# Performance work log

Measured on AMD Instinct MI355X. Metric: run time of the kernel, lower is better.

Reference implementation:

```python
import jax, jax.numpy as jnp
import numpy as np
import math

N_VERT = 35709
N_FACE = 70789
BATCH = 32


def _normalize(x, axis=-1, eps=1e-12):
    n = jnp.linalg.norm(x, axis=axis, keepdims=True)
    return x / jnp.maximum(n, eps)


def setup_inputs() -> dict:
    key = jax.random.key(0)
    ks = jax.random.split(key, 9)
    coeff = jax.random.normal(ks[0], (BATCH, 277), jnp.float32)
    idBase = jax.random.normal(ks[1], (3 * N_VERT, 80), jnp.float32)
    exBase = jax.random.normal(ks[2], (3 * N_VERT, 64), jnp.float32)
    texBase = jax.random.normal(ks[3], (3 * N_VERT, 100), jnp.float32)
    meanshape = jax.random.normal(ks[4], (3 * N_VERT,), jnp.float32)
    meantex = jax.random.normal(ks[5], (3 * N_VERT,), jnp.float32)
    face_buf = jax.random.randint(ks[6], (N_FACE, 3), 0, N_VERT, jnp.int32)
    # point_buf may index the appended zero-normal row at position N_FACE (padding)
    point_buf = jax.random.randint(ks[7], (N_VERT, 8), 0, N_FACE + 1, jnp.int32)
    keypoints = jax.random.randint(ks[8], (68,), 0, N_VERT, jnp.int32)
    return dict(coeff=coeff, idBase=idBase, exBase=exBase, texBase=texBase,
                meanshape=meanshape, meantex=meantex, face_buf=face_buf,
                point_buf=point_buf, keypoints=keypoints)


def reference(coeff, idBase, exBase, texBase, meanshape, meantex,
              face_buf, point_buf, keypoints):
    B = coeff.shape[0]
    # ---- Split_coeff (canonical 80/64/100/3/27/3 layout) ----
    id_c = coeff[:, :80]
    ex_c = coeff[:, 80:144]
    tex_c = coeff[:, 144:244]
    angles = coeff[:, 244:247]
    gamma = coeff[:, 247:274]
    trans = coeff[:, 274:277]
    cam_scale = jnp.ones((B, 1), coeff.dtype)
    f_scale = jnp.ones((B, 1), coeff.dtype)

    # ---- Shape formation ----
    fs = (jnp.einsum('ij,aj->ai', idBase, id_c)
          + jnp.einsum('ij,aj->ai', exBase, ex_c)
          + meanshape[None, :])
    fs = fs.reshape(B, -1, 3)  # [B, N, 3]
    fs = fs - jnp.mean(meanshape.reshape(-1, 3), axis=0)[None, None, :]

    # ---- Texture formation ----
    tex = (jnp.einsum('ij,aj->ai', texBase, tex_c) + meantex[None, :]).reshape(B, -1, 3)

    # ---- Rotation matrix (Rz @ Ry @ Rx, then transpose) ----
    cx, sx = jnp.cos(angles[:, 0]), jnp.sin(angles[:, 0])
    cy, sy = jnp.cos(angles[:, 1]), jnp.sin(angles[:, 1])
    cz, sz = jnp.cos(angles[:, 2]), jnp.sin(angles[:, 2])
    o, z = jnp.ones_like(cx), jnp.zeros_like(cx)
    Rx = jnp.stack([o, z, z, z, cx, -sx, z, sx, cx], -1).reshape(B, 3, 3)
    Ry = jnp.stack([cy, z, sy, z, o, z, -sy, z, cy], -1).reshape(B, 3, 3)
    Rz = jnp.stack([cz, -sz, z, sz, cz, z, z, z, o], -1).reshape(B, 3, 3)
    rot = jnp.swapaxes(jnp.matmul(jnp.matmul(Rz, Ry), Rx), 1, 2)  # [B,3,3]

    # ---- Compute_norm: gather face verts, cross, aggregate to vertices ----
    v1 = fs[:, face_buf[:, 0], :]  # [B, F, 3]
    v2 = fs[:, face_buf[:, 1], :]
    v3 = fs[:, face_buf[:, 2], :]
    face_norm = _normalize(jnp.cross(v1 - v2, v2 - v3), axis=2)  # [B, F, 3]
    face_norm = jnp.concatenate(
        [face_norm, jnp.zeros((B, 1, 3), face_norm.dtype)], axis=1)  # pad row
    v_norm = _normalize(jnp.sum(face_norm[:, point_buf, :], axis=2), axis=2)  # [B,N,3]

    norm_r = jnp.matmul(v_norm, rot)

    # ---- Rigid transform + landmarks ----
    fst = jnp.matmul(fs, rot) + trans[:, None, :]
    lm = fst[:, keypoints, :]  # [B, 68, 3]

    # ---- Projection block (applied to landmarks) ----
    focal = 1015.0 * f_scale  # [B,1]
    camera_pos = jnp.array([0.0, 0.0, 10.0], coeff.dtype) * cam_scale[:, :, None]  # [B,1,3]
    reverse_z = jnp.diag(jnp.array([1.0, 1.0, -1.0], coeff.dtype))
    z1 = jnp.zeros((B, 1), coeff.dtype)
    z2 = jnp.zeros((B, 2), coeff.dtype)
    o1 = jnp.ones((B, 1), coeff.dtype)
    p_matrix = jnp.concatenate(
        [focal, z1, 112.0 * o1, z1, focal, 112.0 * o1, z2, o1], axis=1).reshape(B, 3, 3)
    lm_cam = jnp.matmul(lm, reverse_z[None]) + camera_pos
    aug = jnp.matmul(lm_cam, jnp.swapaxes(p_matrix, 1, 2))
    landmark_p = aug[..., :2] / aug[..., 2:3]

    # ---- SH illumination ----
    init_lit = jnp.array([0.8, 0, 0, 0, 0, 0, 0, 0, 0], coeff.dtype)
    g = gamma.reshape(B, 3, 9) + init_lit[None, None, :]
    pi = math.pi
    a0, a1, a2 = pi, 2 * pi / math.sqrt(3.0), 2 * pi / math.sqrt(8.0)
    c0 = 1.0 / math.sqrt(4 * pi)
    c1 = math.sqrt(3.0) / math.sqrt(4 * pi)
    c2 = 3 * math.sqrt(5.0) / math.sqrt(12 * pi)
    nx, ny, nz = norm_r[..., 0], norm_r[..., 1], norm_r[..., 2]
    Y = jnp.stack([
        a0 * c0 * jnp.ones_like(nx),
        -a1 * c1 * ny,
        a1 * c1 * nz,
        -a1 * c1 * nx,
        a2 * c2 * nx * ny,
        -a2 * c2 * ny * nz,
        a2 * c2 * 0.5 / math.sqrt(3.0) * (3 * nz * nz - 1),
        -a2 * c2 * nx * nz,
        a2 * c2 * 0.5 * (nx * nx - ny * ny),
    ], axis=-1)  # [B, N, 9]
    lighting = jnp.einsum('bnk,bck->bnc', Y, g)  # [B, N, 3]
    face_color = tex * lighting

    return face_color, landmark_p, fst
```

## Files before the change

### kernel.cpp

```cpp
#include <hip/hip_runtime.h>

#define N_VERT 35709
#define N_FACE 70789
#define NB 32
#define M3 (3*N_VERT)

#define WS_FS4X  ((size_t)0)
#define WS_FN4X  (WS_FS4X + (size_t)N_VERT*128)
#define WS_CPAD  (WS_FN4X + (size_t)(N_FACE+1)*128)
#define WS_ROT   (WS_CPAD + (size_t)NB*256)
#define WS_TRE   (WS_ROT + (size_t)NB*9)
#define WS_G     (WS_TRE + (size_t)NB*3)
#define WS_MEAN  (WS_G + (size_t)NB*27)

#define FC_OFF   ((size_t)0)
#define LM_OFF   ((size_t)NB*M3)
#define FST_OFF  (LM_OFF + (size_t)NB*68*2)

#define A0C0 0.88622692545275801f
#define A1C1 1.77245385090551603f
#define A2C2 2.42703239430f
#define Y6C  0.70062393935f
#define Y8C  1.21351619715f

__global__ void __launch_bounds__(256) face3d_stageA1(
    const float* __restrict__ ms, float* __restrict__ ws) {
  float s0=0.f, s1=0.f, s2=0.f;
  for (int v = blockIdx.x*256 + threadIdx.x; v < N_VERT; v += gridDim.x*256) {
    s0 += ms[3*v+0]; s1 += ms[3*v+1]; s2 += ms[3*v+2];
  }
  #pragma unroll
  for (int off = 32; off > 0; off >>= 1) {
    s0 += __shfl_down(s0, off);
    s1 += __shfl_down(s1, off);
    s2 += __shfl_down(s2, off);
  }
  if ((threadIdx.x & 63) == 0) {
    atomicAdd(&ws[WS_MEAN+0], s0);
    atomicAdd(&ws[WS_MEAN+1], s1);
    atomicAdd(&ws[WS_MEAN+2], s2);
  }
}

__global__ void __launch_bounds__(256) face3d_stageA2(
    const float* __restrict__ coeff, float* __restrict__ ws) {
  int t = threadIdx.x;
  float m0 = ws[WS_MEAN+0]*(1.0f/N_VERT);
  float m1 = ws[WS_MEAN+1]*(1.0f/N_VERT);
  float m2 = ws[WS_MEAN+2]*(1.0f/N_VERT);
  float4* cp4 = (float4*)(ws + WS_CPAD);
  for (int idx = t; idx < 64*32; idx += 256) {
    int s4 = idx >> 5, b = idx & 31;
    int k = 4*s4;
    float4 v;
    v.x = (k < 244) ? coeff[b*277 + k + 0] : 0.f;
    v.y = (k < 244) ? coeff[b*277 + k + 1] : 0.f;
    v.z = (k < 244) ? coeff[b*277 + k + 2] : 0.f;
    v.w = (k < 244) ? coeff[b*277 + k + 3] : 0.f;
    cp4[idx] = v;
  }
  for (int idx = t; idx < NB*27; idx += 256) {
    int b = idx / 27, k = idx - b*27;
    ws[WS_G + idx] = coeff[b*277 + 247 + k] + (((k % 9) == 0) ? 0.8f : 0.0f);
  }
  if (t < NB) {
    int b = t;
    float ax = coeff[b*277+244], ay = coeff[b*277+245], az = coeff[b*277+246];
    float cx=cosf(ax), sx=sinf(ax);
    float cy=cosf(ay), sy=sinf(ay);
    float cz=cosf(az), sz=sinf(az);
    float T00=cz*cy, T01=-sz, T02=cz*sy;
    float T10=sz*cy, T11=cz,  T12=sz*sy;
    float T20=-sy,   T21=0.f, T22=cy;
    float R[3][3];
    R[0][0]=T00; R[0][1]=T01*cx+T02*sx; R[0][2]=-T01*sx+T02*cx;
    R[1][0]=T10; R[1][1]=T11*cx+T12*sx; R[1][2]=-T11*sx+T12*cx;
    R[2][0]=T20; R[2][1]=T21*cx+T22*sx; R[2][2]=-T21*sx+T22*cx;
    float rot[3][3];
    #pragma unroll
    for (int c=0;c<3;c++)
      #pragma unroll
      for (int j=0;j<3;j++)
        rot[c][j] = R[j][c];
    #pragma unroll
    for (int c=0;c<3;c++)
      #pragma unroll
      for (int j=0;j<3;j++)
        ws[WS_ROT + b*9 + c*3 + j] = rot[c][j];
    #pragma unroll
    for (int j=0;j<3;j++)
      ws[WS_TRE + b*3 + j] = coeff[b*277+274+j]
        - (m0*rot[0][j] + m1*rot[1][j] + m2*rot[2][j]);
  }
}


template<int NK4, int SOFF>
__device__ __forceinline__ void gemm2(const float4* __restrict__ A0,
                                      const float4* __restrict__ A1,
                                      const float4* __restrict__ Wl,
                                      float acc[2][NB]) {
  float4 c0 = A0[0], c1 = A1[0];
  #pragma unroll 1
  for (int s = 0; s < NK4; ++s) {
    float4 a0 = c0, a1 = c1;
    if (s + 1 < NK4) { c0 = A0[s+1]; c1 = A1[s+1]; }
    const float4* __restrict__ Ws = Wl + (size_t)(SOFF + s)*32;
    #pragma unroll
    for (int b = 0; b < NB; ++b) {
      float4 w = Ws[b];
      acc[0][b] = fmaf(a0.w, w.w, fmaf(a0.z, w.z, fmaf(a0.y, w.y, fmaf(a0.x, w.x, acc[0][b]))));
      acc[1][b] = fmaf(a1.w, w.w, fmaf(a1.z, w.z, fmaf(a1.y, w.y, fmaf(a1.x, w.x, acc[1][b]))));
    }
  }
}

__global__ void __launch_bounds__(128) face3d_stageB(
    const float* __restrict__ idB, const float* __restrict__ exB,
    const float* __restrict__ texB, const float* __restrict__ meanshape,
    const float* __restrict__ meantex, const float* __restrict__ cpadT,
    float* __restrict__ fs4x, float* __restrict__ texOut) {
  __shared__ float4 Wl[36*32];
  int t = threadIdx.x;
  int bid = blockIdx.x;
  int isTex = bid & 1;
  int r0 = (bid >> 1) * 256;

  const float4* __restrict__ cp4 = (const float4*)cpadT;
  if (!isTex) {
    #pragma unroll
    for (int i = 0; i < 9; ++i) Wl[t + 128*i] = cp4[t + 128*i];
  } else {
    for (int i = t; i < 25*32; i += 128) Wl[i] = cp4[36*32 + i];
  }
  __syncthreads();

  int ra = r0 + t;
  int rb = r0 + t + 128;
  int rac = (ra < M3) ? ra : (M3-1);
  int rbc = (rb < M3) ? rb : (M3-1);

  float acc[2][NB];
  #pragma unroll
  for (int j = 0; j < 2; ++j)
    #pragma unroll
    for (int b = 0; b < NB; ++b) acc[j][b] = 0.f;

  if (!isTex) {
    gemm2<20, 0 >((const float4*)idB + (size_t)rac*20,
                  (const float4*)idB + (size_t)rbc*20, Wl, acc);
    gemm2<16, 20>((const float4*)exB + (size_t)rac*16,
                  (const float4*)exB + (size_t)rbc*16, Wl, acc);
    #pragma unroll
    for (int j = 0; j < 2; ++j) {
      int r = (j == 0) ? ra : rb;
      if (r < M3) {
        float msv = meanshape[r];
        int v = r/3, c = r - 3*v;
        float* dst = fs4x + (size_t)v*128 + c;
        #pragma unroll
        for (int b = 0; b < NB; ++b) dst[b*4] = acc[j][b] + msv;
      }
    }
  } else {
    gemm2<25, 0 >((const float4*)texB + (size_t)rac*25,
                  (const float4*)texB + (size_t)rbc*25, Wl, acc);
    #pragma unroll
    for (int j = 0; j < 2; ++j) {
      int r = (j == 0) ? ra : rb;
      if (r < M3) {
        float mtv = meantex[r];
        #pragma unroll
        for (int b = 0; b < NB; ++b) texOut[(size_t)b*M3 + r] = acc[j][b] + mtv;
      }
    }
  }
}

__global__ void __launch_bounds__(256) face3d_stageC(
    const int* __restrict__ face_buf, const float* __restrict__ fs4x,
    float* __restrict__ fn4x) {
  int t = threadIdx.x;
  int b = t & 31, fi = t >> 5;
  int f = blockIdx.x*8 + fi;
  if (f > N_FACE) return;
  float4* o = (float4*)(fn4x + ((size_t)f*32 + b)*4);
  if (f == N_FACE) { *o = make_float4(0.f,0.f,0.f,0.f); return; }
  int i0 = face_buf[f*3+0];
  int i1 = face_buf[f*3+1];
  int i2 = face_buf[f*3+2];
  float4 p1 = *(const float4*)(fs4x + ((size_t)i0*32 + b)*4);
  float4 p2 = *(const float4*)(fs4x + ((size_t)i1*32 + b)*4);
  float4 p3 = *(const float4*)(fs4x + ((size_t)i2*32 + b)*4);
  float e1x = p1.x-p2.x, e1y = p1.y-p2.y, e1z = p1.z-p2.z;
  float e2x = p2.x-p3.x, e2y = p2.y-p3.y, e2z = p2.z-p3.z;
  float nx = e1y*e2z - e1z*e2y;
  float ny = e1z*e2x - e1x*e2z;
  float nz = e1x*e2y - e1y*e2x;
  float inv = 1.0f / fmaxf(sqrtf(nx*nx + ny*ny + nz*nz), 1e-12f);
  *o = make_float4(nx*inv, ny*inv, nz*inv, 0.f);
}

__global__ void __launch_bounds__(256) face3d_stageD(
    const int* __restrict__ point_buf, const int* __restrict__ keypoints,
    const float* __restrict__ fs4x, const float* __restrict__ fn4x,
    const float* __restrict__ rotAll, const float* __restrict__ treAll,
    const float* __restrict__ gAll, float* __restrict__ out) {
  const int mainBlocks = (N_VERT + 7)/8;
  int bid = blockIdx.x;
  int t = threadIdx.x;
  if (bid < mainBlocks) {
    __shared__ float rotL[NB*9];
    __shared__ float treL[NB*3];
    __shared__ float gL[NB*27];
    __shared__ float fstL[NB*33];
    __shared__ float LL[NB*33];
    if (t < NB*9)  rotL[t] = rotAll[t];
    if (t < NB*3)  treL[t] = treAll[t];
    for (int i = t; i < NB*27; i += 256) gL[i] = gAll[i];
    __syncthreads();
    int b = t & 31, vi = t >> 5;
    int v0 = bid*8;
    int v = v0 + vi;
    if (v < N_VERT) {
      const int4 pb0 = *(const int4*)(point_buf + (size_t)v*8);
      const int4 pb1 = *(const int4*)(point_buf + (size_t)v*8 + 4);
      float4 g0 = *(const float4*)(fn4x + ((size_t)pb0.x*32 + b)*4);
      float4 g1 = *(const float4*)(fn4x + ((size_t)pb0.y*32 + b)*4);
      float4 g2 = *(const float4*)(fn4x + ((size_t)pb0.z*32 + b)*4);
      float4 g3 = *(const float4*)(fn4x + ((size_t)pb0.w*32 + b)*4);
      float4 g4 = *(const float4*)(fn4x + ((size_t)pb1.x*32 + b)*4);
      float4 g5 = *(const float4*)(fn4x + ((size_t)pb1.y*32 + b)*4);
      float4 g6 = *(const float4*)(fn4x + ((size_t)pb1.z*32 + b)*4);
      float4 g7 = *(const float4*)(fn4x + ((size_t)pb1.w*32 + b)*4);
      float sx = ((g0.x+g1.x)+(g2.x+g3.x)) + ((g4.x+g5.x)+(g6.x+g7.x));
      float sy = ((g0.y+g1.y)+(g2.y+g3.y)) + ((g4.y+g5.y)+(g6.y+g7.y));
      float sz = ((g0.z+g1.z)+(g2.z+g3.z)) + ((g4.z+g5.z)+(g6.z+g7.z));
      float inv = 1.0f / fmaxf(sqrtf(sx*sx + sy*sy + sz*sz), 1e-12f);
      float n0 = sx*inv, n1 = sy*inv, n2 = sz*inv;
      const float* rot = rotL + b*9;
      float r00=rot[0], r01=rot[1], r02=rot[2];
      float r10=rot[3], r11=rot[4], r12=rot[5];
      float r20=rot[6], r21=rot[7], r22=rot[8];
      float nx = n0*r00 + n1*r10 + n2*r20;
      float ny = n0*r01 + n1*r11 + n2*r21;
      float nz = n0*r02 + n1*r12 + n2*r22;
      float Y1 = -A1C1*ny;
      float Y2 =  A1C1*nz;
      float Y3 = -A1C1*nx;
      float Y4 =  A2C2*nx*ny;
      float Y5 = -A2C2*ny*nz;
      float Y6 =  Y6C*(3.f*nz*nz - 1.f);
      float Y7 = -A2C2*nx*nz;
      float Y8 =  Y8C*(nx*nx - ny*ny);
      const float* g = gL + b*27;
      #pragma unroll
      for (int c = 0; c < 3; ++c) {
        const float* gc = g + c*9;
        float Lc = A0C0*gc[0] + Y1*gc[1] + Y2*gc[2] + Y3*gc[3] + Y4*gc[4]
                 + Y5*gc[5] + Y6*gc[6] + Y7*gc[7] + Y8*gc[8];
        LL[b*33 + vi*4 + c] = Lc;
      }
      float4 fsv = *(const float4*)(fs4x + ((size_t)v*32 + b)*4);
      const float* tre = treL + b*3;
      fstL[b*33 + vi*4 + 0] = fsv.x*r00 + fsv.y*r10 + fsv.z*r20 + tre[0];
      fstL[b*33 + vi*4 + 1] = fsv.x*r01 + fsv.y*r11 + fsv.z*r21 + tre[1];
      fstL[b*33 + vi*4 + 2] = fsv.x*r02 + fsv.y*r12 + fsv.z*r22 + tre[2];
    }
    __syncthreads();
    int b2 = t >> 3, w = t & 7;
    if (v0 + w < N_VERT) {
      size_t obase = (size_t)b2*M3 + (size_t)(v0 + w)*3;
      float f0 = fstL[b2*33 + w*4 + 0];
      float f1 = fstL[b2*33 + w*4 + 1];
      float f2 = fstL[b2*33 + w*4 + 2];
      out[FST_OFF + obase + 0] = f0;
      out[FST_OFF + obase + 1] = f1;
      out[FST_OFF + obase + 2] = f2;
      float l0 = LL[b2*33 + w*4 + 0];
      float l1 = LL[b2*33 + w*4 + 1];
      float l2 = LL[b2*33 + w*4 + 2];
      float t0 = out[FC_OFF + obase + 0];
      float t1 = out[FC_OFF + obase + 1];
      float t2 = out[FC_OFF + obase + 2];
      out[FC_OFF + obase + 0] = t0*l0;
      out[FC_OFF + obase + 1] = t1*l1;
      out[FC_OFF + obase + 2] = t2*l2;
    }
  } else {
    int idx = (bid - mainBlocks)*256 + t;
    if (idx >= NB*68) return;
    int b = idx & 31, j = idx >> 5;
    int kp = keypoints[j];
    const float* rot = rotAll + b*9;
    const float* tre = treAll + b*3;
    float4 fsv = *(const float4*)(fs4x + ((size_t)kp*32 + b)*4);
    float o0 = fsv.x*rot[0] + fsv.y*rot[3] + fsv.z*rot[6] + tre[0];
    float o1 = fsv.x*rot[1] + fsv.y*rot[4] + fsv.z*rot[7] + tre[1];
    float o2 = fsv.x*rot[2] + fsv.y*rot[5] + fsv.z*rot[8] + tre[2];
    float zc = 10.0f - o2;
    float axv = 1015.0f*o0 + 112.0f*zc;
    float ayv = 1015.0f*o1 + 112.0f*zc;
    out[LM_OFF + (size_t)b*136 + (size_t)j*2 + 0] = axv/zc;
    out[LM_OFF + (size_t)b*136 + (size_t)j*2 + 1] = ayv/zc;
  }
}

extern "C" void kernel_launch(void* const* d_in, const int* in_sizes, int n_in,
                              void* d_out, int out_size, void* d_ws, size_t ws_size,
                              hipStream_t stream) {
  const float* coeff     = (const float*)d_in[0];
  const float* idB       = (const float*)d_in[1];
  const float* exB       = (const float*)d_in[2];
  const float* texB      = (const float*)d_in[3];
  const float* meanshape = (const float*)d_in[4];
  const float* meantex   = (const float*)d_in[5];
  const int*   face_buf  = (const int*)d_in[6];
  const int*   point_buf = (const int*)d_in[7];
  const int*   keypoints = (const int*)d_in[8];
  float* out = (float*)d_out;
  float* ws  = (float*)d_ws;

  hipMemsetAsync((char*)d_ws + WS_MEAN*sizeof(float), 0, 3*sizeof(float), stream);

  hipLaunchKernelGGL(face3d_stageA1, dim3(56), dim3(256), 0, stream, meanshape, ws);
  hipLaunchKernelGGL(face3d_stageA2, dim3(1), dim3(256), 0, stream, coeff, ws);

  int gridB = 2 * ((M3 + 255)/256);
  hipLaunchKernelGGL(face3d_stageB, dim3(gridB), dim3(128), 0, stream,
                     idB, exB, texB, meanshape, meantex,
                     ws + WS_CPAD, ws + WS_FS4X, out + FC_OFF);

  int gridC = (N_FACE + 1 + 7)/8;
  hipLaunchKernelGGL(face3d_stageC, dim3(gridC), dim3(256), 0, stream,
                     face_buf, ws + WS_FS4X, ws + WS_FN4X);

  int mainBlocks = (N_VERT + 7)/8;
  int lmBlocks   = (NB*68 + 255)/256;
  hipLaunchKernelGGL(face3d_stageD, dim3(mainBlocks + lmBlocks), dim3(256), 0, stream,
                     point_buf, keypoints, ws + WS_FS4X, ws + WS_FN4X,
                     ws + WS_ROT, ws + WS_TRE, ws + WS_G, out);
}
```

Baseline: 278.2 us.

## Fuse face-normal computation into per-vertex normal kernel, drop stage C

Removes the separate face-normal kernel and its intermediate buffer. Each vertex thread now recomputes the normals of its 8 adjacent faces directly from the face indices and vertex positions. This saves one launch plus the write and re-read of a (N_FACE+1)x32 float4 buffer. In exchange it triples the random gathers per adjacent face (3 vertex float4 loads instead of 1 normal load) and repeats the cross-product work about 8x/2 times, since each face is shared by roughly 3.4 vertices.

```diff
diff --git a/kernel.cpp b/kernel.cpp
--- a/kernel.cpp
+++ b/kernel.cpp
@@ -177,33 +177,10 @@
   }
 }
 
-__global__ void __launch_bounds__(256) face3d_stageC(
-    const int* __restrict__ face_buf, const float* __restrict__ fs4x,
-    float* __restrict__ fn4x) {
-  int t = threadIdx.x;
-  int b = t & 31, fi = t >> 5;
-  int f = blockIdx.x*8 + fi;
-  if (f > N_FACE) return;
-  float4* o = (float4*)(fn4x + ((size_t)f*32 + b)*4);
-  if (f == N_FACE) { *o = make_float4(0.f,0.f,0.f,0.f); return; }
-  int i0 = face_buf[f*3+0];
-  int i1 = face_buf[f*3+1];
-  int i2 = face_buf[f*3+2];
-  float4 p1 = *(const float4*)(fs4x + ((size_t)i0*32 + b)*4);
-  float4 p2 = *(const float4*)(fs4x + ((size_t)i1*32 + b)*4);
-  float4 p3 = *(const float4*)(fs4x + ((size_t)i2*32 + b)*4);
-  float e1x = p1.x-p2.x, e1y = p1.y-p2.y, e1z = p1.z-p2.z;
-  float e2x = p2.x-p3.x, e2y = p2.y-p3.y, e2z = p2.z-p3.z;
-  float nx = e1y*e2z - e1z*e2y;
-  float ny = e1z*e2x - e1x*e2z;
-  float nz = e1x*e2y - e1y*e2x;
-  float inv = 1.0f / fmaxf(sqrtf(nx*nx + ny*ny + nz*nz), 1e-12f);
-  *o = make_float4(nx*inv, ny*inv, nz*inv, 0.f);
-}
-
 __global__ void __launch_bounds__(256) face3d_stageD(
-    const int* __restrict__ point_buf, const int* __restrict__ keypoints,
-    const float* __restrict__ fs4x, const float* __restrict__ fn4x,
+    const int* __restrict__ face_buf, const int* __restrict__ point_buf,
+    const int* __restrict__ keypoints,
+    const float* __restrict__ fs4x,
     const float* __restrict__ rotAll, const float* __restrict__ treAll,
     const float* __restrict__ gAll, float* __restrict__ out) {
   const int mainBlocks = (N_VERT + 7)/8;
@@ -225,17 +202,31 @@
     if (v < N_VERT) {
       const int4 pb0 = *(const int4*)(point_buf + (size_t)v*8);
       const int4 pb1 = *(const int4*)(point_buf + (size_t)v*8 + 4);
-      float4 g0 = *(const float4*)(fn4x + ((size_t)pb0.x*32 + b)*4);
-      float4 g1 = *(const float4*)(fn4x + ((size_t)pb0.y*32 + b)*4);
-      float4 g2 = *(const float4*)(fn4x + ((size_t)pb0.z*32 + b)*4);
-      float4 g3 = *(const float4*)(fn4x + ((size_t)pb0.w*32 + b)*4);
-      float4 g4 = *(const float4*)(fn4x + ((size_t)pb1.x*32 + b)*4);
-      float4 g5 = *(const float4*)(fn4x + ((size_t)pb1.y*32 + b)*4);
-      float4 g6 = *(const float4*)(fn4x + ((size_t)pb1.z*32 + b)*4);
-      float4 g7 = *(const float4*)(fn4x + ((size_t)pb1.w*32 + b)*4);
-      float sx = ((g0.x+g1.x)+(g2.x+g3.x)) + ((g4.x+g5.x)+(g6.x+g7.x));
-      float sy = ((g0.y+g1.y)+(g2.y+g3.y)) + ((g4.y+g5.y)+(g6.y+g7.y));
-      float sz = ((g0.z+g1.z)+(g2.z+g3.z)) + ((g4.z+g5.z)+(g6.z+g7.z));
+      int fk[8] = {pb0.x, pb0.y, pb0.z, pb0.w, pb1.x, pb1.y, pb1.z, pb1.w};
+      float nxk[8], nyk[8], nzk[8];
+      #pragma unroll
+      for (int k = 0; k < 8; ++k) {
+        int f = fk[k];
+        float rx = 0.f, ry = 0.f, rz = 0.f;
+        if (f != N_FACE) {
+          const int* fb = face_buf + (size_t)f*3;
+          int i0 = fb[0], i1 = fb[1], i2 = fb[2];
+          float4 p1 = *(const float4*)(fs4x + ((size_t)i0*32 + b)*4);
+          float4 p2 = *(const float4*)(fs4x + ((size_t)i1*32 + b)*4);
+          float4 p3 = *(const float4*)(fs4x + ((size_t)i2*32 + b)*4);
+          float e1x = p1.x-p2.x, e1y = p1.y-p2.y, e1z = p1.z-p2.z;
+          float e2x = p2.x-p3.x, e2y = p2.y-p3.y, e2z = p2.z-p3.z;
+          float cxv = e1y*e2z - e1z*e2y;
+          float cyv = e1z*e2x - e1x*e2z;
+          float czv = e1x*e2y - e1y*e2x;
+          float inv = 1.0f / fmaxf(sqrtf(cxv*cxv + cyv*cyv + czv*czv), 1e-12f);
+          rx = cxv*inv; ry = cyv*inv; rz = czv*inv;
+        }
+        nxk[k] = rx; nyk[k] = ry; nzk[k] = rz;
+      }
+      float sx = ((nxk[0]+nxk[1])+(nxk[2]+nxk[3])) + ((nxk[4]+nxk[5])+(nxk[6]+nxk[7]));
+      float sy = ((nyk[0]+nyk[1])+(nyk[2]+nyk[3])) + ((nyk[4]+nyk[5])+(nyk[6]+nyk[7]));
+      float sz = ((nzk[0]+nzk[1])+(nzk[2]+nzk[3])) + ((nzk[4]+nzk[5])+(nzk[6]+nzk[7]));
       float inv = 1.0f / fmaxf(sqrtf(sx*sx + sy*sy + sz*sz), 1e-12f);
       float n0 = sx*inv, n1 = sy*inv, n2 = sz*inv;
       const float* rot = rotL + b*9;
@@ -331,13 +322,9 @@
                      idB, exB, texB, meanshape, meantex,
                      ws + WS_CPAD, ws + WS_FS4X, out + FC_OFF);
 
-  int gridC = (N_FACE + 1 + 7)/8;
-  hipLaunchKernelGGL(face3d_stageC, dim3(gridC), dim3(256), 0, stream,
-                     face_buf, ws + WS_FS4X, ws + WS_FN4X);
-
   int mainBlocks = (N_VERT + 7)/8;
   int lmBlocks   = (NB*68 + 255)/256;
   hipLaunchKernelGGL(face3d_stageD, dim3(mainBlocks + lmBlocks), dim3(256), 0, stream,
-                     point_buf, keypoints, ws + WS_FS4X, ws + WS_FN4X,
+                     face_buf, point_buf, keypoints, ws + WS_FS4X,
                      ws + WS_ROT, ws + WS_TRE, ws + WS_G, out);
 }
```

New measurement: 289.7 us. 4.1% more time.

## Fuse texture GEMM into vertex stage and drop tex round-trip through output

Applied to the files above, without the earlier changes.

Removes the texture half of the basis GEMM kernel and instead computes each vertex's three texture rows inside the per-vertex lighting kernel, using tex coefficients staged in shared memory. This avoids writing the full batched texture to the output buffer and reading it back to multiply by lighting. In exchange the per-vertex kernel gains a 100-term dot product per thread and extra shared memory, which may reduce occupancy and GEMM efficiency.

```diff
diff --git a/kernel.cpp b/kernel.cpp
--- a/kernel.cpp
+++ b/kernel.cpp
@@ -117,22 +117,15 @@
 
 __global__ void __launch_bounds__(128) face3d_stageB(
     const float* __restrict__ idB, const float* __restrict__ exB,
-    const float* __restrict__ texB, const float* __restrict__ meanshape,
-    const float* __restrict__ meantex, const float* __restrict__ cpadT,
-    float* __restrict__ fs4x, float* __restrict__ texOut) {
+    const float* __restrict__ meanshape, const float* __restrict__ cpadT,
+    float* __restrict__ fs4x) {
   __shared__ float4 Wl[36*32];
   int t = threadIdx.x;
-  int bid = blockIdx.x;
-  int isTex = bid & 1;
-  int r0 = (bid >> 1) * 256;
+  int r0 = blockIdx.x * 256;
 
   const float4* __restrict__ cp4 = (const float4*)cpadT;
-  if (!isTex) {
-    #pragma unroll
-    for (int i = 0; i < 9; ++i) Wl[t + 128*i] = cp4[t + 128*i];
-  } else {
-    for (int i = t; i < 25*32; i += 128) Wl[i] = cp4[36*32 + i];
-  }
+  #pragma unroll
+  for (int i = 0; i < 9; ++i) Wl[t + 128*i] = cp4[t + 128*i];
   __syncthreads();
 
   int ra = r0 + t;
@@ -146,33 +139,19 @@
     #pragma unroll
     for (int b = 0; b < NB; ++b) acc[j][b] = 0.f;
 
-  if (!isTex) {
-    gemm2<20, 0 >((const float4*)idB + (size_t)rac*20,
-                  (const float4*)idB + (size_t)rbc*20, Wl, acc);
-    gemm2<16, 20>((const float4*)exB + (size_t)rac*16,
-                  (const float4*)exB + (size_t)rbc*16, Wl, acc);
-    #pragma unroll
-    for (int j = 0; j < 2; ++j) {
-      int r = (j == 0) ? ra : rb;
-      if (r < M3) {
-        float msv = meanshape[r];
-        int v = r/3, c = r - 3*v;
-        float* dst = fs4x + (size_t)v*128 + c;
-        #pragma unroll
-        for (int b = 0; b < NB; ++b) dst[b*4] = acc[j][b] + msv;
-      }
-    }
-  } else {
-    gemm2<25, 0 >((const float4*)texB + (size_t)rac*25,
-                  (const float4*)texB + (size_t)rbc*25, Wl, acc);
-    #pragma unroll
-    for (int j = 0; j < 2; ++j) {
-      int r = (j == 0) ? ra : rb;
-      if (r < M3) {
-        float mtv = meantex[r];
-        #pragma unroll
-        for (int b = 0; b < NB; ++b) texOut[(size_t)b*M3 + r] = acc[j][b] + mtv;
-      }
+  gemm2<20, 0 >((const float4*)idB + (size_t)rac*20,
+                (const float4*)idB + (size_t)rbc*20, Wl, acc);
+  gemm2<16, 20>((const float4*)exB + (size_t)rac*16,
+                (const float4*)exB + (size_t)rbc*16, Wl, acc);
+  #pragma unroll
+  for (int j = 0; j < 2; ++j) {
+    int r = (j == 0) ? ra : rb;
+    if (r < M3) {
+      float msv = meanshape[r];
+      int v = r/3, c = r - 3*v;
+      float* dst = fs4x + (size_t)v*128 + c;
+      #pragma unroll
+      for (int b = 0; b < NB; ++b) dst[b*4] = acc[j][b] + msv;
     }
   }
 }
@@ -204,6 +183,8 @@
 __global__ void __launch_bounds__(256) face3d_stageD(
     const int* __restrict__ point_buf, const int* __restrict__ keypoints,
     const float* __restrict__ fs4x, const float* __restrict__ fn4x,
+    const float* __restrict__ texB, const float* __restrict__ meantex,
+    const float* __restrict__ cpadT,
     const float* __restrict__ rotAll, const float* __restrict__ treAll,
     const float* __restrict__ gAll, float* __restrict__ out) {
   const int mainBlocks = (N_VERT + 7)/8;
@@ -215,9 +196,15 @@
     __shared__ float gL[NB*27];
     __shared__ float fstL[NB*33];
     __shared__ float LL[NB*33];
+    __shared__ float texL[NB*33];
+    __shared__ float4 Wt[25*32];
     if (t < NB*9)  rotL[t] = rotAll[t];
     if (t < NB*3)  treL[t] = treAll[t];
     for (int i = t; i < NB*27; i += 256) gL[i] = gAll[i];
+    {
+      const float4* __restrict__ cp4 = (const float4*)cpadT;
+      for (int i = t; i < 25*32; i += 256) Wt[i] = cp4[36*32 + i];
+    }
     __syncthreads();
     int b = t & 31, vi = t >> 5;
     int v0 = bid*8;
@@ -266,26 +253,35 @@
       fstL[b*33 + vi*4 + 0] = fsv.x*r00 + fsv.y*r10 + fsv.z*r20 + tre[0];
       fstL[b*33 + vi*4 + 1] = fsv.x*r01 + fsv.y*r11 + fsv.z*r21 + tre[1];
       fstL[b*33 + vi*4 + 2] = fsv.x*r02 + fsv.y*r12 + fsv.z*r22 + tre[2];
+      {
+        const float4* __restrict__ T4 = (const float4*)texB;
+        size_t rbase = (size_t)(3*v) * 25;
+        float a0 = 0.f, a1 = 0.f, a2 = 0.f;
+        #pragma unroll 5
+        for (int s = 0; s < 25; ++s) {
+          float4 w  = Wt[s*32 + b];
+          float4 x0 = T4[rbase + s];
+          float4 x1 = T4[rbase + 25 + s];
+          float4 x2 = T4[rbase + 50 + s];
+          a0 = fmaf(x0.w, w.w, fmaf(x0.z, w.z, fmaf(x0.y, w.y, fmaf(x0.x, w.x, a0))));
+          a1 = fmaf(x1.w, w.w, fmaf(x1.z, w.z, fmaf(x1.y, w.y, fmaf(x1.x, w.x, a1))));
+          a2 = fmaf(x2.w, w.w, fmaf(x2.z, w.z, fmaf(x2.y, w.y, fmaf(x2.x, w.x, a2))));
+        }
+        texL[b*33 + vi*4 + 0] = a0 + meantex[3*v + 0];
+        texL[b*33 + vi*4 + 1] = a1 + meantex[3*v + 1];
+        texL[b*33 + vi*4 + 2] = a2 + meantex[3*v + 2];
+      }
     }
     __syncthreads();
     int b2 = t >> 3, w = t & 7;
     if (v0 + w < N_VERT) {
       size_t obase = (size_t)b2*M3 + (size_t)(v0 + w)*3;
-      float f0 = fstL[b2*33 + w*4 + 0];
-      float f1 = fstL[b2*33 + w*4 + 1];
-      float f2 = fstL[b2*33 + w*4 + 2];
-      out[FST_OFF + obase + 0] = f0;
-      out[FST_OFF + obase + 1] = f1;
-      out[FST_OFF + obase + 2] = f2;
-      float l0 = LL[b2*33 + w*4 + 0];
-      float l1 = LL[b2*33 + w*4 + 1];
-      float l2 = LL[b2*33 + w*4 + 2];
-      float t0 = out[FC_OFF + obase + 0];
-      float t1 = out[FC_OFF + obase + 1];
-      float t2 = out[FC_OFF + obase + 2];
-      out[FC_OFF + obase + 0] = t0*l0;
-      out[FC_OFF + obase + 1] = t1*l1;
-      out[FC_OFF + obase + 2] = t2*l2;
+      out[FST_OFF + obase + 0] = fstL[b2*33 + w*4 + 0];
+      out[FST_OFF + obase + 1] = fstL[b2*33 + w*4 + 1];
+      out[FST_OFF + obase + 2] = fstL[b2*33 + w*4 + 2];
+      out[FC_OFF + obase + 0] = texL[b2*33 + w*4 + 0] * LL[b2*33 + w*4 + 0];
+      out[FC_OFF + obase + 1] = texL[b2*33 + w*4 + 1] * LL[b2*33 + w*4 + 1];
+      out[FC_OFF + obase + 2] = texL[b2*33 + w*4 + 2] * LL[b2*33 + w*4 + 2];
     }
   } else {
     int idx = (bid - mainBlocks)*256 + t;
@@ -326,10 +322,9 @@
   hipLaunchKernelGGL(face3d_stageA1, dim3(56), dim3(256), 0, stream, meanshape, ws);
   hipLaunchKernelGGL(face3d_stageA2, dim3(1), dim3(256), 0, stream, coeff, ws);
 
-  int gridB = 2 * ((M3 + 255)/256);
+  int gridB = (M3 + 255)/256;
   hipLaunchKernelGGL(face3d_stageB, dim3(gridB), dim3(128), 0, stream,
-                     idB, exB, texB, meanshape, meantex,
-                     ws + WS_CPAD, ws + WS_FS4X, out + FC_OFF);
+                     idB, exB, meanshape, ws + WS_CPAD, ws + WS_FS4X);
 
   int gridC = (N_FACE + 1 + 7)/8;
   hipLaunchKernelGGL(face3d_stageC, dim3(gridC), dim3(256), 0, stream,
@@ -339,5 +334,6 @@
   int lmBlocks   = (NB*68 + 255)/256;
   hipLaunchKernelGGL(face3d_stageD, dim3(mainBlocks + lmBlocks), dim3(256), 0, stream,
                      point_buf, keypoints, ws + WS_FS4X, ws + WS_FN4X,
+                     texB, meantex, ws + WS_CPAD,
                      ws + WS_ROT, ws + WS_TRE, ws + WS_G, out);
 }
```

New measurement: 301.1 us. 8.2% more time.
